# Performance work log

Measured on AMD Instinct MI355X. Metric: run time of the kernel, lower is better.

The kernel has to match this reference:

```python
import jax, jax.numpy as jnp
import numpy as np

TEMPERATURE = 0.5
EPS = 1e-8
NEG = -1e30  # effectively -inf for masked logits


def _l2norm(x):
    n = jnp.sqrt(jnp.sum(x * x, axis=1, keepdims=True))
    return x / jnp.maximum(n, EPS)


def setup_inputs() -> dict:
    key = jax.random.key(0)
    ks = jax.random.split(key, 4)
    N, D = 2048, 128
    return {f"projection_image_aug{i+1}": jax.random.normal(ks[i], (N, D), dtype=jnp.float32)
            for i in range(4)}


def reference(projection_image_aug1, projection_image_aug2,
              projection_image_aug3, projection_image_aug4):
    zs = [projection_image_aug1.astype(jnp.float32),
          projection_image_aug2.astype(jnp.float32),
          projection_image_aug3.astype(jnp.float32),
          projection_image_aug4.astype(jnp.float32)]
    N = zs[0].shape[0]
    k = len(zs)
    z = jnp.concatenate(zs[:2], axis=0)        # [2N, D]
    z_all = jnp.concatenate(zs, axis=0)        # [kN, D]
    # cosine sim via normalize + matmul (same math as broadcast CosineSimilarity)
    sim = _l2norm(z) @ _l2norm(z_all).T / TEMPERATURE   # [2N, kN]

    rows = jnp.arange(2 * N)
    half = rows // N                 # 0 for first N rows, 1 for second
    idx = rows % N
    cols = jnp.arange(k * N)
    block = cols // N
    # mask: diagonal entries of every N-block except the target block (1-half)
    diag = (cols[None, :] % N) == idx[:, None]
    mask = diag & (block[None, :] != (1 - half)[:, None])
    sim_m = jnp.where(mask, NEG, sim)
    # positive column: aug2 partner for rows<N, aug1 partner for rows>=N
    target_col = (1 - half) * N + idx
    pos = jnp.take_along_axis(sim_m, target_col[:, None], axis=1)[:, 0]
    # cross_entropy(reduction='sum') / (2N)
    loss = jnp.sum(jax.nn.logsumexp(sim_m, axis=1) - pos) / (2 * N)
    return loss
```

## Files before the change

kernel.cpp:

```cpp
#include <hip/hip_runtime.h>
#include <hip/hip_bf16.h>


#define NN      2048
#define DD      128
#define TWO_N   4096
#define FOUR_N  8192
#define BM      128
#define BN      128
#define CT      64

using frag_ab = __attribute__((ext_vector_type(8))) short;
using f32x4   = __attribute__((ext_vector_type(4))) float;

__device__ inline void gl_lds16(const short* g, short* l) {
  __builtin_amdgcn_global_load_lds(
      (const __attribute__((address_space(1))) void*)g,
      (__attribute__((address_space(3))) void*)l, 16, 0, 0);
}

__global__ __launch_bounds__(256) void knorm(const float* __restrict__ p0,
                                             const float* __restrict__ p1,
                                             const float* __restrict__ p2,
                                             const float* __restrict__ p3,
                                             short* __restrict__ Bn,
                                             float* __restrict__ out) {
  if (blockIdx.x == 0 && threadIdx.x == 0) out[0] = 0.0f;
  int wave = threadIdx.x >> 6, lane = threadIdx.x & 63;
  int row = blockIdx.x * 4 + wave;
  int q = row >> 11, idx = row & (NN - 1);
  const float* src = (q == 0) ? p0 : (q == 1) ? p1 : (q == 2) ? p2 : p3;
  const float2* s2 = (const float2*)(src + (size_t)idx * DD);
  float2 v = s2[lane];
  float ss = v.x * v.x + v.y * v.y;
  #pragma unroll
  for (int sh = 1; sh < 64; sh <<= 1) ss += __shfl_xor(ss, sh, 64);
  float inv = 1.0f / fmaxf(sqrtf(ss), 1e-8f);
  __hip_bfloat162 o;
  o.x = __float2bfloat16(v.x * inv);
  o.y = __float2bfloat16(v.y * inv);
  ((__hip_bfloat162*)(Bn + (size_t)row * DD))[lane] = o;
}

__global__ __launch_bounds__(256) void kgemm(const short* __restrict__ Bn,
                                             float2* __restrict__ pMS) {
  __shared__ short sA[BM * DD];
  __shared__ short sB[BN * DD];
  __shared__ float sM[BM][2];
  __shared__ float sS[BM][2];

  int t = threadIdx.x, wave = t >> 6, lane = t & 63;
  int quad = lane >> 4, l16 = lane & 15;

  const short* gA = Bn + (size_t)blockIdx.x * BM * DD;
  const short* gB = Bn + (size_t)blockIdx.y * BN * DD;
  #pragma unroll
  for (int i = 0; i < 8; ++i) {
    int c0 = i * 256 + wave * 64;
    gl_lds16(gA + (size_t)(c0 + lane) * 8, sA + (size_t)c0 * 8);
    gl_lds16(gB + (size_t)(c0 + lane) * 8, sB + (size_t)c0 * 8);
  }
  __syncthreads();

  int rowHalf = wave >> 1, colHalf = wave & 1;
  f32x4 acc[4][4];
  #pragma unroll
  for (int rf = 0; rf < 4; ++rf)
    #pragma unroll
    for (int cf = 0; cf < 4; ++cf) acc[rf][cf] = (f32x4){0.f, 0.f, 0.f, 0.f};

  #pragma unroll
  for (int k = 0; k < 4; ++k) {
    frag_ab a[4], b[4];
    #pragma unroll
    for (int rf = 0; rf < 4; ++rf)
      a[rf] = *(const frag_ab*)&sA[(rowHalf * 64 + rf * 16 + l16) * DD + k * 32 + quad * 8];
    #pragma unroll
    for (int cf = 0; cf < 4; ++cf)
      b[cf] = *(const frag_ab*)&sB[(colHalf * 64 + cf * 16 + l16) * DD + k * 32 + quad * 8];
    #pragma unroll
    for (int rf = 0; rf < 4; ++rf)
      #pragma unroll
      for (int cf = 0; cf < 4; ++cf)
        acc[rf][cf] = __builtin_amdgcn_mfma_f32_16x16x32_bf16(a[rf], b[cf], acc[rf][cf], 0, 0, 0);
  }

  int grBase = blockIdx.x * BM;
  int colBase = blockIdx.y * BN + colHalf * 64;
  #pragma unroll
  for (int rf = 0; rf < 4; ++rf) {
    #pragma unroll
    for (int r = 0; r < 4; ++r) {
      int rowLocal = rowHalf * 64 + rf * 16 + quad * 4 + r;
      int gr = grBase + rowLocal;
      int idx = gr & (NN - 1);
      int notblk = 1 - (gr >> 11);
      float vals[4];
      float m = -1e30f;
      #pragma unroll
      for (int cf = 0; cf < 4; ++cf) {
        int c = colBase + cf * 16 + l16;
        float v = acc[rf][cf][r] * 2.0f;
        bool masked = ((c & (NN - 1)) == idx) && ((c >> 11) != notblk);
        v = masked ? -1e30f : v;
        vals[cf] = v;
        m = fmaxf(m, v);
      }
      #pragma unroll
      for (int sh = 1; sh < 16; sh <<= 1) m = fmaxf(m, __shfl_xor(m, sh, 64));
      float s = 0.f;
      #pragma unroll
      for (int cf = 0; cf < 4; ++cf) s += __expf(vals[cf] - m);
      #pragma unroll
      for (int sh = 1; sh < 16; sh <<= 1) s += __shfl_xor(s, sh, 64);
      if (l16 == 0) { sM[rowLocal][colHalf] = m; sS[rowLocal][colHalf] = s; }
    }
  }
  __syncthreads();
  if (t < BM) {
    float m0 = sM[t][0], m1 = sM[t][1];
    float s0 = sS[t][0], s1 = sS[t][1];
    float M = fmaxf(m0, m1);
    float S = s0 * __expf(m0 - M) + s1 * __expf(m1 - M);
    pMS[(size_t)blockIdx.y * TWO_N + grBase + t] = make_float2(M, S);
  }
}

__global__ __launch_bounds__(1024) void krow(const short* __restrict__ Bn,
                                             const float2* __restrict__ pMS,
                                             float* __restrict__ out) {
  int t = threadIdx.x, w = t >> 6, lane = t & 63;
  int gr = blockIdx.x * 16 + w;
  float2 p = pMS[(size_t)lane * TWO_N + gr];
  float M = p.x;
  #pragma unroll
  for (int sh = 1; sh < 64; sh <<= 1) M = fmaxf(M, __shfl_xor(M, sh, 64));
  float S = p.y * __expf(p.x - M);
  #pragma unroll
  for (int sh = 1; sh < 64; sh <<= 1) S += __shfl_xor(S, sh, 64);
  float lse = M + __logf(S);

  int idx = gr & (NN - 1), half = gr >> 11;
  int tgt = (1 - half) * NN + idx;
  unsigned int ua = ((const unsigned int*)(Bn + (size_t)gr * DD))[lane];
  unsigned int ub = ((const unsigned int*)(Bn + (size_t)tgt * DD))[lane];
  float a0 = __uint_as_float((ua & 0xffffu) << 16);
  float a1 = __uint_as_float(ua & 0xffff0000u);
  float b0 = __uint_as_float((ub & 0xffffu) << 16);
  float b1 = __uint_as_float(ub & 0xffff0000u);
  float dot = a0 * b0 + a1 * b1;
  #pragma unroll
  for (int sh = 1; sh < 64; sh <<= 1) dot += __shfl_xor(dot, sh, 64);
  float loss = lse - 2.0f * dot;

  __shared__ float wsum[16];
  if (lane == 0) wsum[w] = loss;
  __syncthreads();
  if (t == 0) {
    float s = 0.f;
    #pragma unroll
    for (int i = 0; i < 16; ++i) s += wsum[i];
    atomicAdd(out, s * (1.0f / (float)TWO_N));
  }
}

extern "C" void kernel_launch(void* const* d_in, const int* in_sizes, int n_in,
                              void* d_out, int out_size, void* d_ws, size_t ws_size,
                              hipStream_t stream) {
  (void)in_sizes; (void)n_in; (void)out_size; (void)ws_size;
  const float* p0 = (const float*)d_in[0];
  const float* p1 = (const float*)d_in[1];
  const float* p2 = (const float*)d_in[2];
  const float* p3 = (const float*)d_in[3];

  short* Bn = (short*)d_ws;
  float2* pMS = (float2*)((char*)d_ws + (size_t)FOUR_N * DD * sizeof(short));
  float* out = (float*)d_out;

  knorm<<<FOUR_N / 4, 256, 0, stream>>>(p0, p1, p2, p3, Bn, out);
  kgemm<<<dim3(TWO_N / BM, FOUR_N / BN), 256, 0, stream>>>(Bn, pMS);
  krow<<<TWO_N / 16, 1024, 0, stream>>>(Bn, pMS, out);
}
```

Measured before the change: 111.1 us.

## Fuse row reduction into GEMM via last-block counter, fixed-max softmax, swizzled LDS

Drops the separate row-reduction kernel: each GEMM block writes partial exp-sums, and the last block per row tile (found with an atomic counter) computes the logsumexp and the positive term. Because the rows are unit-normalized, the max-subtraction and masking are replaced by a fixed shift of 2. The masked diagonal terms are subtracted afterwards using recomputed self and cross dot products. An XOR swizzle of the LDS layout is added to cut bank conflicts on the fragment loads. This saves a launch and the shuffle-max work, but relies on the fixed bound and subtraction being accurate enough, and adds threadfence and atomic overhead.

```diff
diff --git a/kernel.cpp b/kernel.cpp
--- a/kernel.cpp
+++ b/kernel.cpp
@@ -19,13 +19,21 @@
       (__attribute__((address_space(3))) void*)l, 16, 0, 0);
 }
 
+__device__ inline int swz(int chunk) {
+  return (chunk & ~15) | ((chunk & 15) ^ ((chunk >> 4) & 15));
+}
+
 __global__ __launch_bounds__(256) void knorm(const float* __restrict__ p0,
                                              const float* __restrict__ p1,
                                              const float* __restrict__ p2,
                                              const float* __restrict__ p3,
                                              short* __restrict__ Bn,
+                                             int* __restrict__ cnt,
                                              float* __restrict__ out) {
-  if (blockIdx.x == 0 && threadIdx.x == 0) out[0] = 0.0f;
+  if (blockIdx.x == 0) {
+    if (threadIdx.x < 32) cnt[threadIdx.x] = 0;
+    if (threadIdx.x == 32) out[0] = 0.0f;
+  }
   int wave = threadIdx.x >> 6, lane = threadIdx.x & 63;
   int row = blockIdx.x * 4 + wave;
   int q = row >> 11, idx = row & (NN - 1);
@@ -43,11 +51,14 @@
 }
 
 __global__ __launch_bounds__(256) void kgemm(const short* __restrict__ Bn,
-                                             float2* __restrict__ pMS) {
+                                             float* __restrict__ pS,
+                                             int* __restrict__ cnt,
+                                             float* __restrict__ out) {
   __shared__ short sA[BM * DD];
   __shared__ short sB[BN * DD];
-  __shared__ float sM[BM][2];
   __shared__ float sS[BM][2];
+  __shared__ float sRed[4];
+  __shared__ int   isLast;
 
   int t = threadIdx.x, wave = t >> 6, lane = t & 63;
   int quad = lane >> 4, l16 = lane & 15;
@@ -57,8 +68,8 @@
   #pragma unroll
   for (int i = 0; i < 8; ++i) {
     int c0 = i * 256 + wave * 64;
-    gl_lds16(gA + (size_t)(c0 + lane) * 8, sA + (size_t)c0 * 8);
-    gl_lds16(gB + (size_t)(c0 + lane) * 8, sB + (size_t)c0 * 8);
+    gl_lds16(gA + (size_t)swz(c0 + lane) * 8, sA + (size_t)c0 * 8);
+    gl_lds16(gB + (size_t)swz(c0 + lane) * 8, sB + (size_t)c0 * 8);
   }
   __syncthreads();
 
@@ -73,11 +84,15 @@
   for (int k = 0; k < 4; ++k) {
     frag_ab a[4], b[4];
     #pragma unroll
-    for (int rf = 0; rf < 4; ++rf)
-      a[rf] = *(const frag_ab*)&sA[(rowHalf * 64 + rf * 16 + l16) * DD + k * 32 + quad * 8];
+    for (int rf = 0; rf < 4; ++rf) {
+      int r_ = rowHalf * 64 + rf * 16 + l16;
+      a[rf] = *(const frag_ab*)&sA[(size_t)((r_ << 4) | ((k * 4 + quad) ^ l16)) * 8];
+    }
     #pragma unroll
-    for (int cf = 0; cf < 4; ++cf)
-      b[cf] = *(const frag_ab*)&sB[(colHalf * 64 + cf * 16 + l16) * DD + k * 32 + quad * 8];
+    for (int cf = 0; cf < 4; ++cf) {
+      int r_ = colHalf * 64 + cf * 16 + l16;
+      b[cf] = *(const frag_ab*)&sB[(size_t)((r_ << 4) | ((k * 4 + quad) ^ l16)) * 8];
+    }
     #pragma unroll
     for (int rf = 0; rf < 4; ++rf)
       #pragma unroll
@@ -86,82 +101,69 @@
   }
 
   int grBase = blockIdx.x * BM;
-  int colBase = blockIdx.y * BN + colHalf * 64;
   #pragma unroll
   for (int rf = 0; rf < 4; ++rf) {
     #pragma unroll
     for (int r = 0; r < 4; ++r) {
       int rowLocal = rowHalf * 64 + rf * 16 + quad * 4 + r;
-      int gr = grBase + rowLocal;
-      int idx = gr & (NN - 1);
-      int notblk = 1 - (gr >> 11);
-      float vals[4];
-      float m = -1e30f;
-      #pragma unroll
-      for (int cf = 0; cf < 4; ++cf) {
-        int c = colBase + cf * 16 + l16;
-        float v = acc[rf][cf][r] * 2.0f;
-        bool masked = ((c & (NN - 1)) == idx) && ((c >> 11) != notblk);
-        v = masked ? -1e30f : v;
-        vals[cf] = v;
-        m = fmaxf(m, v);
-      }
-      #pragma unroll
-      for (int sh = 1; sh < 16; sh <<= 1) m = fmaxf(m, __shfl_xor(m, sh, 64));
       float s = 0.f;
       #pragma unroll
-      for (int cf = 0; cf < 4; ++cf) s += __expf(vals[cf] - m);
+      for (int cf = 0; cf < 4; ++cf)
+        s += __expf(fmaf(acc[rf][cf][r], 2.0f, -2.0f));
       #pragma unroll
       for (int sh = 1; sh < 16; sh <<= 1) s += __shfl_xor(s, sh, 64);
-      if (l16 == 0) { sM[rowLocal][colHalf] = m; sS[rowLocal][colHalf] = s; }
+      if (l16 == 0) sS[rowLocal][colHalf] = s;
     }
   }
   __syncthreads();
-  if (t < BM) {
-    float m0 = sM[t][0], m1 = sM[t][1];
-    float s0 = sS[t][0], s1 = sS[t][1];
-    float M = fmaxf(m0, m1);
-    float S = s0 * __expf(m0 - M) + s1 * __expf(m1 - M);
-    pMS[(size_t)blockIdx.y * TWO_N + grBase + t] = make_float2(M, S);
+  if (t < BM)
+    pS[(size_t)(grBase + t) * CT + blockIdx.y] = sS[t][0] + sS[t][1];
+
+  __threadfence();
+  if (t == 0) {
+    int old = atomicAdd(&cnt[blockIdx.x], 1);
+    isLast = (old == (int)gridDim.y - 1);
   }
-}
+  __syncthreads();
+  if (!isLast) return;
+  __threadfence();
 
-__global__ __launch_bounds__(1024) void krow(const short* __restrict__ Bn,
-                                             const float2* __restrict__ pMS,
-                                             float* __restrict__ out) {
-  int t = threadIdx.x, w = t >> 6, lane = t & 63;
-  int gr = blockIdx.x * 16 + w;
-  float2 p = pMS[(size_t)lane * TWO_N + gr];
-  float M = p.x;
-  #pragma unroll
-  for (int sh = 1; sh < 64; sh <<= 1) M = fmaxf(M, __shfl_xor(M, sh, 64));
-  float S = p.y * __expf(p.x - M);
-  #pragma unroll
-  for (int sh = 1; sh < 64; sh <<= 1) S += __shfl_xor(S, sh, 64);
-  float lse = M + __logf(S);
-
-  int idx = gr & (NN - 1), half = gr >> 11;
-  int tgt = (1 - half) * NN + idx;
-  unsigned int ua = ((const unsigned int*)(Bn + (size_t)gr * DD))[lane];
-  unsigned int ub = ((const unsigned int*)(Bn + (size_t)tgt * DD))[lane];
-  float a0 = __uint_as_float((ua & 0xffffu) << 16);
-  float a1 = __uint_as_float(ua & 0xffff0000u);
-  float b0 = __uint_as_float((ub & 0xffffu) << 16);
-  float b1 = __uint_as_float(ub & 0xffff0000u);
-  float dot = a0 * b0 + a1 * b1;
-  #pragma unroll
-  for (int sh = 1; sh < 64; sh <<= 1) dot += __shfl_xor(dot, sh, 64);
-  float loss = lse - 2.0f * dot;
-
-  __shared__ float wsum[16];
-  if (lane == 0) wsum[w] = loss;
+  float wloss = 0.f;
+  for (int rr = wave; rr < BM; rr += 4) {
+    int gr = grBase + rr;
+    int idx = gr & (NN - 1), half = gr >> 11;
+    float S = pS[(size_t)gr * CT + lane];
+    #pragma unroll
+    for (int sh = 1; sh < 64; sh <<= 1) S += __shfl_xor(S, sh, 64);
+    unsigned int ua = ((const unsigned int*)(Bn + (size_t)gr * DD))[lane];
+    unsigned int ub = ((const unsigned int*)(Bn + (size_t)((1 - half) * NN + idx) * DD))[lane];
+    unsigned int uc = ((const unsigned int*)(Bn + (size_t)(2 * NN + idx) * DD))[lane];
+    unsigned int ud = ((const unsigned int*)(Bn + (size_t)(3 * NN + idx) * DD))[lane];
+    float a0 = __uint_as_float((ua & 0xffffu) << 16), a1 = __uint_as_float(ua & 0xffff0000u);
+    float b0 = __uint_as_float((ub & 0xffffu) << 16), b1 = __uint_as_float(ub & 0xffff0000u);
+    float c0 = __uint_as_float((uc & 0xffffu) << 16), c1 = __uint_as_float(uc & 0xffff0000u);
+    float d0 = __uint_as_float((ud & 0xffffu) << 16), d1 = __uint_as_float(ud & 0xffff0000u);
+    float daa = a0 * a0 + a1 * a1;
+    float dab = a0 * b0 + a1 * b1;
+    float dac = a0 * c0 + a1 * c1;
+    float dad = a0 * d0 + a1 * d1;
+    #pragma unroll
+    for (int sh = 1; sh < 64; sh <<= 1) {
+      daa += __shfl_xor(daa, sh, 64);
+      dab += __shfl_xor(dab, sh, 64);
+      dac += __shfl_xor(dac, sh, 64);
+      dad += __shfl_xor(dad, sh, 64);
+    }
+    float Sc = S - __expf(fmaf(daa, 2.0f, -2.0f))
+                 - __expf(fmaf(dac, 2.0f, -2.0f))
+                 - __expf(fmaf(dad, 2.0f, -2.0f));
+    float loss = (2.0f + __logf(Sc)) - 2.0f * dab;
+    if (lane == 0) wloss += loss;
+  }
+  if (lane == 0) sRed[wave] = wloss;
   __syncthreads();
-  if (t == 0) {
-    float s = 0.f;
-    #pragma unroll
-    for (int i = 0; i < 16; ++i) s += wsum[i];
-    atomicAdd(out, s * (1.0f / (float)TWO_N));
-  }
+  if (t == 0)
+    atomicAdd(out, (sRed[0] + sRed[1] + sRed[2] + sRed[3]) * (1.0f / (float)TWO_N));
 }
 
 extern "C" void kernel_launch(void* const* d_in, const int* in_sizes, int n_in,
@@ -174,10 +176,10 @@
   const float* p3 = (const float*)d_in[3];
 
   short* Bn = (short*)d_ws;
-  float2* pMS = (float2*)((char*)d_ws + (size_t)FOUR_N * DD * sizeof(short));
+  float* pS = (float*)((char*)d_ws + (size_t)FOUR_N * DD * sizeof(short));
+  int* cnt = (int*)(pS + (size_t)TWO_N * CT);
   float* out = (float*)d_out;
 
-  knorm<<<FOUR_N / 4, 256, 0, stream>>>(p0, p1, p2, p3, Bn, out);
-  kgemm<<<dim3(TWO_N / BM, FOUR_N / BN), 256, 0, stream>>>(Bn, pMS);
-  krow<<<TWO_N / 16, 1024, 0, stream>>>(Bn, pMS, out);
+  knorm<<<FOUR_N / 4, 256, 0, stream>>>(p0, p1, p2, p3, Bn, cnt, out);
+  kgemm<<<dim3(TWO_N / BM, FOUR_N / BN), 256, 0, stream>>>(Bn, pS, cnt, out);
 }
```

Result: slower. 308.5 us (+177.6%).
